# Performance work log

Hardware: AMD Instinct MI355X
Metric: run time of the kernel (lower is better)

The kernel has to match this reference:

```python
import jax, jax.numpy as jnp
import numpy as np

FACTOR = 2  # self.factor
KSIZE = 3   # causal_fusion depthwise conv kernel size


def causal_fusion(x, w, b):
    # x: [BH, C, N]; depthwise causal conv over the node axis (left pad k-1)
    k = w.shape[-1]
    out = jax.lax.conv_general_dilated(
        x, w, window_strides=(1,), padding=[(k - 1, 0)],
        dimension_numbers=('NCH', 'OIH', 'NCH'),
        feature_group_count=x.shape[1])
    return out + b[None, :, None]


def setup_inputs() -> dict:
    key = jax.random.key(0)
    ks = jax.random.split(key, 4)
    B, N, L, H, E = 4, 64, 128, 8, 32
    queries = jax.random.normal(ks[0], (B, N, L, H, E), jnp.float32)
    keys = jax.random.normal(ks[1], (B, N, L, H, E), jnp.float32)
    values = jax.random.normal(ks[2], (B, N, L, H, E), jnp.float32)
    attn_mask = jnp.zeros((1,), jnp.bool_)
    C = E * L  # 4096 channels seen by causal_fusion
    w_cf = jax.random.normal(ks[3], (C, 1, KSIZE), jnp.float32) * 0.05
    b_cf = jnp.zeros((C,), jnp.float32)
    return {"queries": queries, "keys": keys, "values": values,
            "attn_mask": attn_mask, "w_cf": w_cf, "b_cf": b_cf}


def reference(queries, keys, values, attn_mask, w_cf, b_cf):
    B, N, L, H, E = queries.shape  # S == L, so no pad/slice branch taken

    # --- FFT cross-correlation: corr[b,n,h,e,:] = irfft(rfft(mean_n q) * conj(rfft(k)))
    qm = jnp.broadcast_to(jnp.mean(queries, axis=1, keepdims=True), queries.shape)
    qp = jnp.transpose(qm, (0, 1, 3, 4, 2))      # [B,N,H,E,L]
    kp = jnp.transpose(keys, (0, 1, 3, 4, 2))    # [B,N,H,E,L]
    vp = jnp.transpose(values, (0, 1, 3, 4, 2))  # [B,N,H,E,L]
    corr = jnp.fft.irfft(jnp.fft.rfft(qp, axis=-1) * jnp.conj(jnp.fft.rfft(kp, axis=-1)), n=L, axis=-1)

    # --- align_speed: top-k delays over channel-mean corr, circular roll of values
    mean_corr = jnp.mean(corr, axis=3)                      # [B,N,H,L]
    weight, delay_idx = jax.lax.top_k(mean_corr, FACTOR)    # [B,N,H,F]
    delay = L - delay_idx                                   # values in [1, L]
    ar = jnp.arange(L)
    aligned = []
    for i in range(FACTOR):
        idx = (ar[None, None, None, None, :] + delay[..., i][..., None, None]) % L  # [B,N,H,1,L]
        idx = jnp.broadcast_to(idx, vp.shape)
        aligned.append(jnp.take_along_axis(vp, idx, axis=-1))  # [B,N,H,E,L]

    BH = B * H
    delay_bh = jnp.transpose(delay, (0, 2, 1, 3)).reshape(BH, N, FACTOR)
    weight_bh = jnp.transpose(weight, (0, 2, 1, 3)).reshape(BH, N, FACTOR)

    # --- per-factor: sort nodes by delay -> causal fusion over nodes -> unsort
    causal_agg = []
    for i in range(FACTOR):
        indices = jnp.argsort(delay_bh[..., i], axis=-1)               # [BH,N]
        av = jnp.transpose(aligned[i], (0, 2, 1, 3, 4)).reshape(BH, N, E, L)
        av = av * jax.nn.sigmoid(weight_bh[..., i])[:, :, None, None]
        sorted_av = jnp.take_along_axis(av, indices[:, :, None, None], axis=1)
        x = jnp.transpose(sorted_av.reshape(BH, N, E * L), (0, 2, 1))  # [BH,E*L,N]
        x = causal_fusion(x, w_cf, b_cf)
        x = jnp.transpose(x, (0, 2, 1)).reshape(BH, N, E, L)
        rev = jnp.argsort(indices, axis=-1)
        x = jnp.take_along_axis(x, rev[:, :, None, None], axis=1)
        causal_agg.append(jnp.transpose(x.reshape(B, H, N, E, L), (0, 2, 1, 3, 4)))  # [B,N,H,E,L]

    # --- align_back_speed: inverse circular shift, mean over factors
    delay_back = L - delay  # [B,N,H,F]
    agg = jnp.zeros_like(causal_agg[0])
    for i in range(FACTOR):
        idx = (ar[None, None, None, None, :] + delay_back[..., i][..., None, None]) % L
        idx = jnp.broadcast_to(idx, causal_agg[i].shape)
        agg = agg + jnp.take_along_axis(causal_agg[i], idx, axis=-1)
    agg = agg / FACTOR

    V = jnp.transpose(agg, (0, 1, 4, 2, 3))  # [B,N,L,H,E]
    return V
```

## Files before the change

### kernel.cpp

```cpp
#include <hip/hip_runtime.h>
#include <math.h>

#define B_ 4
#define N_ 64
#define L_ 128
#define H_ 8
#define E_ 32
#define SC_ 8

typedef __attribute__((ext_vector_type(8))) short short8;
typedef __attribute__((ext_vector_type(4))) float f32x4;

__device__ __forceinline__ unsigned short f2bf(float x) {
    union { float f; unsigned u; } c; c.f = x;
    unsigned r = (c.u + 0x7fffu + ((c.u >> 16) & 1u)) >> 16;
    return (unsigned short)r;
}
__device__ __forceinline__ float bf2f(unsigned short h) {
    union { unsigned u; float f; } c; c.u = ((unsigned)h) << 16;
    return c.f;
}

__global__ __launch_bounds__(256) void k_qmean(const float* __restrict__ q,
                                               float* __restrict__ qm,
                                               const float* __restrict__ w,
                                               const float* __restrict__ bias,
                                               float* __restrict__ wT,
                                               float* __restrict__ bT) {
    int blk = blockIdx.x;
    int b = blk >> 7, t = blk & 127;
    int tid = threadIdx.x;
    int c4 = tid & 63;
    int nq = tid >> 6;
    __shared__ double red[4][256];
    const f32x4* p = (const f32x4*)(q + (((size_t)(b * N_)) * L_ + t) * 256);
    double s0 = 0, s1 = 0, s2 = 0, s3 = 0;
    #pragma unroll 4
    for (int n = nq * 16; n < nq * 16 + 16; ++n) {
        f32x4 v = p[(size_t)n * 8192 + c4];
        s0 += (double)v.x; s1 += (double)v.y; s2 += (double)v.z; s3 += (double)v.w;
    }
    red[nq][c4 * 4 + 0] = s0;
    red[nq][c4 * 4 + 1] = s1;
    red[nq][c4 * 4 + 2] = s2;
    red[nq][c4 * 4 + 3] = s3;
    __syncthreads();
    int c = tid;
    double s = red[0][c] + red[1][c] + red[2][c] + red[3][c];
    qm[((size_t)b * 256 + c) * L_ + t] = (float)(s * (1.0 / 64.0));

    if (blk < 16) {
        int k = blk * 256 + tid;
        int e = k & 31, lp = k >> 5;
        int cc = e * L_ + lp;
        wT[k]        = w[cc * 3 + 0];
        wT[4096 + k] = w[cc * 3 + 1];
        wT[8192 + k] = w[cc * 3 + 2];
        bT[k]        = bias[cc];
    }
}

__global__ __launch_bounds__(512) void k_corr(const float* __restrict__ keys,
                                              const float* __restrict__ qm,
                                              float* __restrict__ part) {
    int blk = blockIdx.x;
    int sc = blk & 7; int bh = blk >> 3; int h = bh & 7; int b = bh >> 3;
    __shared__ unsigned short Ahi[4][64][40];
    __shared__ unsigned short Alo[4][64][40];
    __shared__ unsigned short Qhi[128][40];
    __shared__ unsigned short Qlo[128][40];
    int tid = threadIdx.x;
    int lane = tid & 63, w = tid >> 6;
    int mg = w & 1, ng = w >> 1;

    {
        int e = tid >> 4; int tq = (tid & 15) * 4;
        const float* qp = qm + ((size_t)b * 256 + h * 32 + e) * 128;
        #pragma unroll
        for (int hf = 0; hf < 2; ++hf) {
            int t0 = tq + hf * 64;
            float4 v = *(const float4*)(qp + t0);
            float vv[4] = {v.x, v.y, v.z, v.w};
            #pragma unroll
            for (int j = 0; j < 4; ++j) {
                unsigned short hi = f2bf(vv[j]);
                Qhi[t0 + j][e] = hi;
                Qlo[t0 + j][e] = f2bf(vv[j] - bf2f(hi));
            }
        }
    }
    int sn = tid >> 3; int se = (tid & 7) * 4;
    const float* kbase = keys + ((size_t)(b * N_ + sn) * L_) * 256 + h * 32 + se;
    #pragma unroll
    for (int p = 0; p < 2; ++p) {
        float4 v = *(const float4*)(kbase + (size_t)(sc * 16 + p) * 256);
        float vv[4] = {v.x, v.y, v.z, v.w};
        ushort4 h4, l4;
        unsigned short* hp = (unsigned short*)&h4;
        unsigned short* lp = (unsigned short*)&l4;
        #pragma unroll
        for (int j = 0; j < 4; ++j) {
            hp[j] = f2bf(vv[j]);
            lp[j] = f2bf(vv[j] - bf2f(hp[j]));
        }
        *(ushort4*)&Ahi[p][sn][se] = h4;
        *(ushort4*)&Alo[p][sn][se] = l4;
    }
    __syncthreads();

    f32x4 acc[2][2];
    #pragma unroll
    for (int i = 0; i < 2; ++i)
        #pragma unroll
        for (int j = 0; j < 2; ++j)
            acc[i][j] = (f32x4){0.f, 0.f, 0.f, 0.f};

    int eb = (lane >> 4) * 8;
    int rA0 = (mg * 2) * 16 + (lane & 15);
    int rA1 = rA0 + 16;
    int tau0 = (ng * 2) * 16 + (lane & 15);
    int tau1 = tau0 + 16;

    for (int it = 0; it < 8; ++it) {
        float4 stg0, stg1;
        if (it < 7) {
            stg0 = *(const float4*)(kbase + (size_t)(sc * 16 + 2 * it + 2) * 256);
            stg1 = *(const float4*)(kbase + (size_t)(sc * 16 + 2 * it + 3) * 256);
        }
        #pragma unroll
        for (int sp = 0; sp < 2; ++sp) {
            int p = 2 * it + sp;
            int slot = p & 3;
            int s = sc * 16 + p;
            short8 ah0 = *(const short8*)&Ahi[slot][rA0][eb];
            short8 ah1 = *(const short8*)&Ahi[slot][rA1][eb];
            short8 al0 = *(const short8*)&Alo[slot][rA0][eb];
            short8 al1 = *(const short8*)&Alo[slot][rA1][eb];
            int t0 = (s + tau0) & 127;
            int t1 = (s + tau1) & 127;
            short8 bh0 = *(const short8*)&Qhi[t0][eb];
            short8 bh1 = *(const short8*)&Qhi[t1][eb];
            short8 bl0 = *(const short8*)&Qlo[t0][eb];
            short8 bl1 = *(const short8*)&Qlo[t1][eb];
            acc[0][0] = __builtin_amdgcn_mfma_f32_16x16x32_bf16(ah0, bh0, acc[0][0], 0, 0, 0);
            acc[0][1] = __builtin_amdgcn_mfma_f32_16x16x32_bf16(ah0, bh1, acc[0][1], 0, 0, 0);
            acc[1][0] = __builtin_amdgcn_mfma_f32_16x16x32_bf16(ah1, bh0, acc[1][0], 0, 0, 0);
            acc[1][1] = __builtin_amdgcn_mfma_f32_16x16x32_bf16(ah1, bh1, acc[1][1], 0, 0, 0);
            acc[0][0] = __builtin_amdgcn_mfma_f32_16x16x32_bf16(ah0, bl0, acc[0][0], 0, 0, 0);
            acc[0][1] = __builtin_amdgcn_mfma_f32_16x16x32_bf16(ah0, bl1, acc[0][1], 0, 0, 0);
            acc[1][0] = __builtin_amdgcn_mfma_f32_16x16x32_bf16(ah1, bl0, acc[1][0], 0, 0, 0);
            acc[1][1] = __builtin_amdgcn_mfma_f32_16x16x32_bf16(ah1, bl1, acc[1][1], 0, 0, 0);
            acc[0][0] = __builtin_amdgcn_mfma_f32_16x16x32_bf16(al0, bh0, acc[0][0], 0, 0, 0);
            acc[0][1] = __builtin_amdgcn_mfma_f32_16x16x32_bf16(al0, bh1, acc[0][1], 0, 0, 0);
            acc[1][0] = __builtin_amdgcn_mfma_f32_16x16x32_bf16(al1, bh0, acc[1][0], 0, 0, 0);
            acc[1][1] = __builtin_amdgcn_mfma_f32_16x16x32_bf16(al1, bh1, acc[1][1], 0, 0, 0);
        }
        if (it < 7) {
            #pragma unroll
            for (int sp = 0; sp < 2; ++sp) {
                int p = 2 * it + 2 + sp;
                int slot = p & 3;
                float4 v = sp ? stg1 : stg0;
                float vv[4] = {v.x, v.y, v.z, v.w};
                ushort4 h4, l4;
                unsigned short* hp = (unsigned short*)&h4;
                unsigned short* lp = (unsigned short*)&l4;
                #pragma unroll
                for (int j = 0; j < 4; ++j) {
                    hp[j] = f2bf(vv[j]);
                    lp[j] = f2bf(vv[j] - bf2f(hp[j]));
                }
                *(ushort4*)&Ahi[slot][sn][se] = h4;
                *(ushort4*)&Alo[slot][sn][se] = l4;
            }
        }
        __syncthreads();
    }

    #pragma unroll
    for (int i = 0; i < 2; ++i) {
        int mt = mg * 2 + i;
        #pragma unroll
        for (int j = 0; j < 2; ++j) {
            int nt = ng * 2 + j;
            int tau = nt * 16 + (lane & 15);
            #pragma unroll
            for (int r = 0; r < 4; ++r) {
                int n = mt * 16 + (lane >> 4) * 4 + r;
                part[((((size_t)sc * B_ + b) * N_ + n) * H_ + h) * L_ + tau] = acc[i][j][r];
            }
        }
    }
}

__global__ __launch_bounds__(64) void k_topk(const float* __restrict__ part,
                                             int* __restrict__ didx,
                                             float* __restrict__ sig,
                                             int* __restrict__ flags) {
    int blk = blockIdx.x;
    int lane = threadIdx.x;
    size_t rb = (size_t)blk * L_;
    const size_t stride = (size_t)B_ * N_ * H_ * L_;
    double s0 = 0.0, s1 = 0.0;
    for (int sc = 0; sc < SC_; ++sc) {
        s0 += (double)part[sc * stride + rb + lane];
        s1 += (double)part[sc * stride + rb + lane + 64];
    }
    float v0 = (float)(s0 * (1.0 / 32.0));
    float v1 = (float)(s1 * (1.0 / 32.0));

    float bv = v0; int bi = lane;
    if (v1 > v0) { bv = v1; bi = lane + 64; }
    #pragma unroll
    for (int m = 32; m; m >>= 1) {
        float ov = __shfl_xor(bv, m, 64);
        int   oi = __shfl_xor(bi, m, 64);
        if (ov > bv || (ov == bv && oi < bi)) { bv = ov; bi = oi; }
    }
    int i1 = bi; float w1v = bv;

    float c0 = (lane == i1) ? -INFINITY : v0;
    float c1 = (lane + 64 == i1) ? -INFINITY : v1;
    float bv2 = c0; int bi2 = lane;
    if (c1 > c0) { bv2 = c1; bi2 = lane + 64; }
    #pragma unroll
    for (int m = 32; m; m >>= 1) {
        float ov = __shfl_xor(bv2, m, 64);
        int   oi = __shfl_xor(bi2, m, 64);
        if (ov > bv2 || (ov == bv2 && oi < bi2)) { bv2 = ov; bi2 = oi; }
    }
    int i2 = bi2; float w2v = bv2;

    float d0 = (lane == i1 || lane == i2) ? -INFINITY : v0;
    float d1 = (lane + 64 == i1 || lane + 64 == i2) ? -INFINITY : v1;
    float bv3 = fmaxf(d0, d1);
    #pragma unroll
    for (int m = 32; m; m >>= 1) bv3 = fmaxf(bv3, __shfl_xor(bv3, m, 64));

    if (lane == 0) {
        didx[blk * 2 + 0] = i1;
        didx[blk * 2 + 1] = i2;
        sig[blk * 2 + 0] = 1.f / (1.f + expf(-w1v));
        sig[blk * 2 + 1] = 1.f / (1.f + expf(-w2v));
        flags[blk] = (w2v - bv3 < 1e-3f) ? 1 : 0;
    }
}

__global__ __launch_bounds__(256) void k_fixup(const float* __restrict__ keys,
                                               const float* __restrict__ qm,
                                               const int* __restrict__ flags,
                                               double* __restrict__ vvg) {
    int row = blockIdx.x >> 3; int tg = blockIdx.x & 7;
    if (!flags[row]) return;
    int h = row & 7; int r = row >> 3; int n = r & 63; int b = r >> 6;
    __shared__ float ks_t[L_][E_];
    __shared__ float qs_t[L_][E_];
    __shared__ double red[16][17];
    int tid = threadIdx.x;
    for (int idx = tid; idx < 1024; idx += 256) {
        int s = idx >> 3, e4 = idx & 7;
        *(float4*)&ks_t[s][e4 * 4] =
            *(const float4*)&keys[(((size_t)(b * N_ + n)) * L_ + s) * 256 + h * E_ + e4 * 4];
        int e = idx >> 5, t4 = (idx & 31) * 4;
        float4 v = *(const float4*)&qm[((size_t)b * 256 + h * E_ + e) * L_ + t4];
        float vvj[4] = {v.x, v.y, v.z, v.w};
        #pragma unroll
        for (int j = 0; j < 4; ++j) {
            int t = t4 + j;
            int col = ((((e >> 2) ^ (t & 7)) << 2) | (e & 3));
            qs_t[t][col] = vvj[j];
        }
    }
    __syncthreads();
    int tau = tg * 16 + (tid & 15);
    int g = tid >> 4;
    double a0 = 0, a1 = 0, a2 = 0, a3 = 0, a4 = 0, a5 = 0, a6 = 0, a7 = 0;
    #pragma unroll 2
    for (int s = g * 8; s < g * 8 + 8; ++s) {
        int t = (s + tau) & 127;
        int x = t & 7;
        #pragma unroll
        for (int e4 = 0; e4 < 8; e4 += 2) {
            float4 k0 = *(const float4*)&ks_t[s][e4 * 4];
            float4 k1 = *(const float4*)&ks_t[s][e4 * 4 + 4];
            float4 q0 = *(const float4*)&qs_t[t][(e4 ^ x) << 2];
            float4 q1 = *(const float4*)&qs_t[t][((e4 + 1) ^ x) << 2];
            a0 = fma((double)k0.x, (double)q0.x, a0);
            a1 = fma((double)k0.y, (double)q0.y, a1);
            a2 = fma((double)k0.z, (double)q0.z, a2);
            a3 = fma((double)k0.w, (double)q0.w, a3);
            a4 = fma((double)k1.x, (double)q1.x, a4);
            a5 = fma((double)k1.y, (double)q1.y, a5);
            a6 = fma((double)k1.z, (double)q1.z, a6);
            a7 = fma((double)k1.w, (double)q1.w, a7);
        }
    }
    red[g][tid & 15] = ((a0 + a1) + (a2 + a3)) + ((a4 + a5) + (a6 + a7));
    __syncthreads();
    if (tid < 16) {
        double s = 0;
        #pragma unroll
        for (int gg = 0; gg < 16; ++gg) s += red[gg][tid];
        vvg[(size_t)row * L_ + tg * 16 + tid] = s;
    }
}

__global__ __launch_bounds__(128) void k_sort(int* __restrict__ didx,
                                              float* __restrict__ sig,
                                              const int* __restrict__ flags,
                                              const double* __restrict__ vvg,
                                              int* __restrict__ pred) {
    int bh = blockIdx.x;
    int b = bh >> 3, h = bh & 7;
    int tid = threadIdx.x; int i = tid >> 6; int n = tid & 63;
    __shared__ int ds[2][64];
    __shared__ int pm[2][64];
    ds[i][n] = 128 - didx[((b * 64 + n) * 8 + h) * 2 + i];
    __syncthreads();

    if (tid < 64) {
        int lane = tid;
        int myflag = flags[(b * 64 + lane) * 8 + h];
        unsigned long long msk = __ballot(myflag != 0);
        while (msk) {
            int nn = __ffsll((long long)msk) - 1; msk &= msk - 1;
            int row = (b * 64 + nn) * 8 + h;
            float v0 = (float)(vvg[(size_t)row * L_ + lane] * (1.0 / 32.0));
            float v1 = (float)(vvg[(size_t)row * L_ + lane + 64] * (1.0 / 32.0));
            float bv = v0; int bi = lane;
            if (v1 > v0) { bv = v1; bi = lane + 64; }
            #pragma unroll
            for (int m = 32; m; m >>= 1) {
                float ov = __shfl_xor(bv, m, 64);
                int   oi = __shfl_xor(bi, m, 64);
                if (ov > bv || (ov == bv && oi < bi)) { bv = ov; bi = oi; }
            }
            int i1 = bi; float w1v = bv;
            float c0 = (lane == i1) ? -INFINITY : v0;
            float c1 = (lane + 64 == i1) ? -INFINITY : v1;
            float bv2 = c0; int bi2 = lane;
            if (c1 > c0) { bv2 = c1; bi2 = lane + 64; }
            #pragma unroll
            for (int m = 32; m; m >>= 1) {
                float ov = __shfl_xor(bv2, m, 64);
                int   oi = __shfl_xor(bi2, m, 64);
                if (ov > bv2 || (ov == bv2 && oi < bi2)) { bv2 = ov; bi2 = oi; }
            }
            if (lane == 0) {
                didx[row * 2 + 0] = i1;
                didx[row * 2 + 1] = bi2;
                sig[row * 2 + 0] = 1.f / (1.f + expf(-w1v));
                sig[row * 2 + 1] = 1.f / (1.f + expf(-bv2));
                ds[0][nn] = 128 - i1;
                ds[1][nn] = 128 - bi2;
            }
        }
    }
    __syncthreads();

    int d = ds[i][n];
    int rank = 0;
    for (int m = 0; m < 64; ++m) {
        int dm = ds[i][m];
        rank += (dm < d || (dm == d && m < n)) ? 1 : 0;
    }
    pm[i][rank] = n;
    __syncthreads();
    int p1v = (rank >= 1) ? pm[i][rank - 1] : -1;
    int p2v = (rank >= 2) ? pm[i][rank - 2] : -1;
    int o = ((bh * 2 + i) * 64 + n) * 2;
    pred[o] = p1v; pred[o + 1] = p2v;
}

__global__ __launch_bounds__(256, 2) void k_out(const float* __restrict__ values,
                                                const float* __restrict__ wT,
                                                const float* __restrict__ bT,
                                                const int* __restrict__ didx,
                                                const float* __restrict__ sig,
                                                const int* __restrict__ pred,
                                                float* __restrict__ out) {
    int bid = blockIdx.x;
    int h = bid & 7;
    int b = bid >> 10;
    int j = (bid >> 3) & 127;
    int n = j >> 1; int half = j & 1;
    int blk = (b * 64 + n) * 8 + h;
    int tid = threadIdx.x; int e4 = tid & 7; int tq = tid >> 3;

    int di[2]; float si[2];
    int pq1[2], pq2[2], dq1[2], dq2[2]; float s1[2], s2[2];
    #pragma unroll
    for (int i = 0; i < 2; ++i) {
        di[i] = didx[blk * 2 + i];
        si[i] = sig[blk * 2 + i];
        int po = (((b * 8 + h) * 2 + i) * 64 + n) * 2;
        int p1 = pred[po], p2 = pred[po + 1];
        if (p1 >= 0) { int q = ((b * 64 + p1) * 8 + h) * 2 + i; pq1[i] = p1; dq1[i] = didx[q]; s1[i] = sig[q]; }
        else         { pq1[i] = n; dq1[i] = di[i]; s1[i] = 0.f; }
        if (p2 >= 0) { int q = ((b * 64 + p2) * 8 + h) * 2 + i; pq2[i] = p2; dq2[i] = didx[q]; s2[i] = sig[q]; }
        else         { pq2[i] = n; dq2[i] = di[i]; s2[i] = 0.f; }
    }
    const f32x4* v4 = (const f32x4*)values;
    const f32x4* w4 = (const f32x4*)wT;
    const f32x4* b4 = (const f32x4*)bT;
    f32x4* o4 = (f32x4*)out;
    const size_t base = ((size_t)b * N_) * L_ * 64 + h * 8 + e4;

    f32x4 vs[2], va1[2], va2[2], vb1[2], vb2[2];
    int lp0[2], lp1[2];
    #pragma unroll
    for (int it = 0; it < 2; ++it) {
        int t = half * 64 + tq + 32 * it;
        vs[it] = v4[base + ((size_t)n * L_ + t) * 64];
        int ta1 = (t + di[0] - dq1[0]) & 127;
        va1[it] = v4[base + ((size_t)pq1[0] * L_ + ta1) * 64];
        int ta2 = (t + di[0] - dq2[0]) & 127;
        va2[it] = v4[base + ((size_t)pq2[0] * L_ + ta2) * 64];
        int tb1 = (t + di[1] - dq1[1]) & 127;
        vb1[it] = v4[base + ((size_t)pq1[1] * L_ + tb1) * 64];
        int tb2 = (t + di[1] - dq2[1]) & 127;
        vb2[it] = v4[base + ((size_t)pq2[1] * L_ + tb2) * 64];
        lp0[it] = (t + di[0]) & 127;
        lp1[it] = (t + di[1]) & 127;
    }
    f32x4 bb0[2], w0a[2], w1a[2], w2a[2], bb1[2], w0b[2], w1b[2], w2b[2];
    #pragma unroll
    for (int it = 0; it < 2; ++it) {
        int wo0 = lp0[it] * 8 + e4, wo1 = lp1[it] * 8 + e4;
        bb0[it] = b4[wo0]; w0a[it] = w4[wo0]; w1a[it] = w4[1024 + wo0]; w2a[it] = w4[2048 + wo0];
        bb1[it] = b4[wo1]; w0b[it] = w4[wo1]; w1b[it] = w4[1024 + wo1]; w2b[it] = w4[2048 + wo1];
    }
    #pragma unroll
    for (int it = 0; it < 2; ++it) {
        int t = half * 64 + tq + 32 * it;
        f32x4 acc = bb0[it] + bb1[it];
        acc += w2a[it] * (si[0] * vs[it]);
        acc += w1a[it] * (s1[0] * va1[it]);
        acc += w0a[it] * (s2[0] * va2[it]);
        acc += w2b[it] * (si[1] * vs[it]);
        acc += w1b[it] * (s1[1] * vb1[it]);
        acc += w0b[it] * (s2[1] * vb2[it]);
        o4[base + ((size_t)n * L_ + t) * 64] = acc * 0.5f;
    }
}

extern "C" void kernel_launch(void* const* d_in, const int* in_sizes, int n_in,
                              void* d_out, int out_size, void* d_ws, size_t ws_size,
                              hipStream_t stream) {
    const float* queries = (const float*)d_in[0];
    const float* keys    = (const float*)d_in[1];
    const float* values  = (const float*)d_in[2];
    const float* w_cf = (const float*)d_in[4];
    const float* b_cf = (const float*)d_in[5];
    float* out = (float*)d_out;

    float* ws    = (float*)d_ws;
    float* qm    = ws;
    float* wT    = qm + 131072;
    float* bT    = wT + 12288;
    float* sigp  = bT + 4096;
    int*   didxp = (int*)(sigp + 4096);
    int*   predp = didxp + 4096;
    int*   flags = predp + 8192;
    double* vvg  = (double*)(flags + 2048);

    float* part = (float*)d_out;

    k_qmean <<<512,   256, 0, stream>>>(queries, qm, w_cf, b_cf, wT, bT);
    k_corr  <<<256,   512, 0, stream>>>(keys, qm, part);
    k_topk  <<<2048,  64,  0, stream>>>(part, didxp, sigp, flags);
    k_fixup <<<16384, 256, 0, stream>>>(keys, qm, flags, vvg);
    k_sort  <<<32,    128, 0, stream>>>(didxp, sigp, flags, vvg, predp);
    k_out   <<<4096,  256, 0, stream>>>(values, wT, bT, didxp, sigp, predp, out);
}
```

Baseline: 77.27 us.

## Compact fixup work via atomic worklist and precompute per-row gather params

k_topk now appends flagged rows to a global worklist through an atomic counter, and k_fixup runs as a persistent grid of 256 blocks that loops over that list. Previously 16384 blocks were launched and most exited early. k_sort now precomputes each row's predecessor indices, shift deltas and sigmoid weights into packed int4/float4 records, so k_out does one coalesced read per factor instead of chained dependent lookups. k_out is split into 8192 single-iteration blocks with a higher occupancy hint. The costs are an atomic per flagged row and a nondeterministic worklist order, though each vvg entry is still computed independently.

```diff
diff --git a/kernel.cpp b/kernel.cpp
--- a/kernel.cpp
+++ b/kernel.cpp
@@ -26,7 +26,8 @@
                                                const float* __restrict__ w,
                                                const float* __restrict__ bias,
                                                float* __restrict__ wT,
-                                               float* __restrict__ bT) {
+                                               float* __restrict__ bT,
+                                               int* __restrict__ wcnt) {
     int blk = blockIdx.x;
     int b = blk >> 7, t = blk & 127;
     int tid = threadIdx.x;
@@ -58,6 +59,7 @@
         wT[8192 + k] = w[cc * 3 + 2];
         bT[k]        = bias[cc];
     }
+    if (blk == 16 && tid == 0) *wcnt = 0;
 }
 
 __global__ __launch_bounds__(512) void k_corr(const float* __restrict__ keys,
@@ -196,7 +198,9 @@
 __global__ __launch_bounds__(64) void k_topk(const float* __restrict__ part,
                                              int* __restrict__ didx,
                                              float* __restrict__ sig,
-                                             int* __restrict__ flags) {
+                                             int* __restrict__ flags,
+                                             int* __restrict__ wlist,
+                                             int* __restrict__ wcnt) {
     int blk = blockIdx.x;
     int lane = threadIdx.x;
     size_t rb = (size_t)blk * L_;
@@ -242,80 +246,95 @@
         didx[blk * 2 + 1] = i2;
         sig[blk * 2 + 0] = 1.f / (1.f + expf(-w1v));
         sig[blk * 2 + 1] = 1.f / (1.f + expf(-w2v));
-        flags[blk] = (w2v - bv3 < 1e-3f) ? 1 : 0;
+        int fl = (w2v - bv3 < 1e-3f) ? 1 : 0;
+        flags[blk] = fl;
+        if (fl) { int s = atomicAdd(wcnt, 1); wlist[s] = blk; }
     }
 }
 
 __global__ __launch_bounds__(256) void k_fixup(const float* __restrict__ keys,
                                                const float* __restrict__ qm,
-                                               const int* __restrict__ flags,
+                                               const int* __restrict__ wlist,
+                                               const int* __restrict__ wcnt,
                                                double* __restrict__ vvg) {
-    int row = blockIdx.x >> 3; int tg = blockIdx.x & 7;
-    if (!flags[row]) return;
-    int h = row & 7; int r = row >> 3; int n = r & 63; int b = r >> 6;
+    int cnt = *wcnt;
     __shared__ float ks_t[L_][E_];
     __shared__ float qs_t[L_][E_];
     __shared__ double red[16][17];
     int tid = threadIdx.x;
-    for (int idx = tid; idx < 1024; idx += 256) {
-        int s = idx >> 3, e4 = idx & 7;
-        *(float4*)&ks_t[s][e4 * 4] =
-            *(const float4*)&keys[(((size_t)(b * N_ + n)) * L_ + s) * 256 + h * E_ + e4 * 4];
-        int e = idx >> 5, t4 = (idx & 31) * 4;
-        float4 v = *(const float4*)&qm[((size_t)b * 256 + h * E_ + e) * L_ + t4];
-        float vvj[4] = {v.x, v.y, v.z, v.w};
-        #pragma unroll
-        for (int j = 0; j < 4; ++j) {
-            int t = t4 + j;
-            int col = ((((e >> 2) ^ (t & 7)) << 2) | (e & 3));
-            qs_t[t][col] = vvj[j];
-        }
-    }
-    __syncthreads();
-    int tau = tg * 16 + (tid & 15);
-    int g = tid >> 4;
-    double a0 = 0, a1 = 0, a2 = 0, a3 = 0, a4 = 0, a5 = 0, a6 = 0, a7 = 0;
-    #pragma unroll 2
-    for (int s = g * 8; s < g * 8 + 8; ++s) {
-        int t = (s + tau) & 127;
-        int x = t & 7;
-        #pragma unroll
-        for (int e4 = 0; e4 < 8; e4 += 2) {
-            float4 k0 = *(const float4*)&ks_t[s][e4 * 4];
-            float4 k1 = *(const float4*)&ks_t[s][e4 * 4 + 4];
-            float4 q0 = *(const float4*)&qs_t[t][(e4 ^ x) << 2];
-            float4 q1 = *(const float4*)&qs_t[t][((e4 + 1) ^ x) << 2];
-            a0 = fma((double)k0.x, (double)q0.x, a0);
-            a1 = fma((double)k0.y, (double)q0.y, a1);
-            a2 = fma((double)k0.z, (double)q0.z, a2);
-            a3 = fma((double)k0.w, (double)q0.w, a3);
-            a4 = fma((double)k1.x, (double)q1.x, a4);
-            a5 = fma((double)k1.y, (double)q1.y, a5);
-            a6 = fma((double)k1.z, (double)q1.z, a6);
-            a7 = fma((double)k1.w, (double)q1.w, a7);
-        }
-    }
-    red[g][tid & 15] = ((a0 + a1) + (a2 + a3)) + ((a4 + a5) + (a6 + a7));
-    __syncthreads();
-    if (tid < 16) {
-        double s = 0;
-        #pragma unroll
-        for (int gg = 0; gg < 16; ++gg) s += red[gg][tid];
-        vvg[(size_t)row * L_ + tg * 16 + tid] = s;
-    }
-}
-
-__global__ __launch_bounds__(128) void k_sort(int* __restrict__ didx,
-                                              float* __restrict__ sig,
+    for (int wi = blockIdx.x; wi < cnt * 8; wi += gridDim.x) {
+        int row = wlist[wi >> 3]; int tg = wi & 7;
+        int h = row & 7; int r = row >> 3; int n = r & 63; int b = r >> 6;
+        __syncthreads();
+        for (int idx = tid; idx < 1024; idx += 256) {
+            int s = idx >> 3, e4 = idx & 7;
+            *(float4*)&ks_t[s][e4 * 4] =
+                *(const float4*)&keys[(((size_t)(b * N_ + n)) * L_ + s) * 256 + h * E_ + e4 * 4];
+            int e = idx >> 5, t4 = (idx & 31) * 4;
+            float4 v = *(const float4*)&qm[((size_t)b * 256 + h * E_ + e) * L_ + t4];
+            float vvj[4] = {v.x, v.y, v.z, v.w};
+            #pragma unroll
+            for (int j = 0; j < 4; ++j) {
+                int t = t4 + j;
+                int col = ((((e >> 2) ^ (t & 7)) << 2) | (e & 3));
+                qs_t[t][col] = vvj[j];
+            }
+        }
+        __syncthreads();
+        int tau = tg * 16 + (tid & 15);
+        int g = tid >> 4;
+        double a0 = 0, a1 = 0, a2 = 0, a3 = 0, a4 = 0, a5 = 0, a6 = 0, a7 = 0;
+        #pragma unroll 2
+        for (int s = g * 8; s < g * 8 + 8; ++s) {
+            int t = (s + tau) & 127;
+            int x = t & 7;
+            #pragma unroll
+            for (int e4 = 0; e4 < 8; e4 += 2) {
+                float4 k0 = *(const float4*)&ks_t[s][e4 * 4];
+                float4 k1 = *(const float4*)&ks_t[s][e4 * 4 + 4];
+                float4 q0 = *(const float4*)&qs_t[t][(e4 ^ x) << 2];
+                float4 q1 = *(const float4*)&qs_t[t][((e4 + 1) ^ x) << 2];
+                a0 = fma((double)k0.x, (double)q0.x, a0);
+                a1 = fma((double)k0.y, (double)q0.y, a1);
+                a2 = fma((double)k0.z, (double)q0.z, a2);
+                a3 = fma((double)k0.w, (double)q0.w, a3);
+                a4 = fma((double)k1.x, (double)q1.x, a4);
+                a5 = fma((double)k1.y, (double)q1.y, a5);
+                a6 = fma((double)k1.z, (double)q1.z, a6);
+                a7 = fma((double)k1.w, (double)q1.w, a7);
+            }
+        }
+        red[g][tid & 15] = ((a0 + a1) + (a2 + a3)) + ((a4 + a5) + (a6 + a7));
+        __syncthreads();
+        if (tid < 16) {
+            double s = 0;
+            #pragma unroll
+            for (int gg = 0; gg < 16; ++gg) s += red[gg][tid];
+            vvg[(size_t)row * L_ + tg * 16 + tid] = s;
+        }
+    }
+}
+
+__global__ __launch_bounds__(128) void k_sort(const int* __restrict__ didx,
+                                              const float* __restrict__ sig,
                                               const int* __restrict__ flags,
                                               const double* __restrict__ vvg,
-                                              int* __restrict__ pred) {
+                                              int4* __restrict__ gparam_i,
+                                              f32x4* __restrict__ gparam_f) {
     int bh = blockIdx.x;
     int b = bh >> 3, h = bh & 7;
     int tid = threadIdx.x; int i = tid >> 6; int n = tid & 63;
     __shared__ int ds[2][64];
     __shared__ int pm[2][64];
-    ds[i][n] = 128 - didx[((b * 64 + n) * 8 + h) * 2 + i];
+    __shared__ int dival[2][64];
+    __shared__ float sigval[2][64];
+    {
+        int row = (b * 64 + n) * 8 + h;
+        int dv = didx[row * 2 + i];
+        dival[i][n] = dv;
+        sigval[i][n] = sig[row * 2 + i];
+        ds[i][n] = 128 - dv;
+    }
     __syncthreads();
 
     if (tid < 64) {
@@ -347,12 +366,10 @@
                 if (ov > bv2 || (ov == bv2 && oi < bi2)) { bv2 = ov; bi2 = oi; }
             }
             if (lane == 0) {
-                didx[row * 2 + 0] = i1;
-                didx[row * 2 + 1] = bi2;
-                sig[row * 2 + 0] = 1.f / (1.f + expf(-w1v));
-                sig[row * 2 + 1] = 1.f / (1.f + expf(-bv2));
-                ds[0][nn] = 128 - i1;
-                ds[1][nn] = 128 - bi2;
+                dival[0][nn] = i1;      ds[0][nn] = 128 - i1;
+                dival[1][nn] = bi2;     ds[1][nn] = 128 - bi2;
+                sigval[0][nn] = 1.f / (1.f + expf(-w1v));
+                sigval[1][nn] = 1.f / (1.f + expf(-bv2));
             }
         }
     }
@@ -368,80 +385,64 @@
     __syncthreads();
     int p1v = (rank >= 1) ? pm[i][rank - 1] : -1;
     int p2v = (rank >= 2) ? pm[i][rank - 2] : -1;
-    int o = ((bh * 2 + i) * 64 + n) * 2;
-    pred[o] = p1v; pred[o + 1] = p2v;
-}
-
-__global__ __launch_bounds__(256, 2) void k_out(const float* __restrict__ values,
+
+    int din = dival[i][n];
+    int pq1 = (p1v >= 0) ? p1v : n;
+    int pq2 = (p2v >= 0) ? p2v : n;
+    int d1 = (p1v >= 0) ? ((din - dival[i][p1v]) & 127) : 0;
+    int d2 = (p2v >= 0) ? ((din - dival[i][p2v]) & 127) : 0;
+    float s1 = (p1v >= 0) ? sigval[i][p1v] : 0.f;
+    float s2 = (p2v >= 0) ? sigval[i][p2v] : 0.f;
+    int blko = (b * 64 + n) * 8 + h;
+    gparam_i[blko * 2 + i] = make_int4(pq1, pq2, d1, d2);
+    gparam_f[blko * 2 + i] = (f32x4){s1, s2, sigval[i][n], (float)din};
+}
+
+__global__ __launch_bounds__(256, 3) void k_out(const float* __restrict__ values,
                                                 const float* __restrict__ wT,
                                                 const float* __restrict__ bT,
-                                                const int* __restrict__ didx,
-                                                const float* __restrict__ sig,
-                                                const int* __restrict__ pred,
+                                                const int4* __restrict__ gparam_i,
+                                                const f32x4* __restrict__ gparam_f,
                                                 float* __restrict__ out) {
     int bid = blockIdx.x;
     int h = bid & 7;
-    int b = bid >> 10;
-    int j = (bid >> 3) & 127;
-    int n = j >> 1; int half = j & 1;
+    int q = (bid >> 3) & 3;
+    int n = (bid >> 5) & 63;
+    int b = bid >> 11;
     int blk = (b * 64 + n) * 8 + h;
     int tid = threadIdx.x; int e4 = tid & 7; int tq = tid >> 3;
-
-    int di[2]; float si[2];
-    int pq1[2], pq2[2], dq1[2], dq2[2]; float s1[2], s2[2];
-    #pragma unroll
-    for (int i = 0; i < 2; ++i) {
-        di[i] = didx[blk * 2 + i];
-        si[i] = sig[blk * 2 + i];
-        int po = (((b * 8 + h) * 2 + i) * 64 + n) * 2;
-        int p1 = pred[po], p2 = pred[po + 1];
-        if (p1 >= 0) { int q = ((b * 64 + p1) * 8 + h) * 2 + i; pq1[i] = p1; dq1[i] = didx[q]; s1[i] = sig[q]; }
-        else         { pq1[i] = n; dq1[i] = di[i]; s1[i] = 0.f; }
-        if (p2 >= 0) { int q = ((b * 64 + p2) * 8 + h) * 2 + i; pq2[i] = p2; dq2[i] = didx[q]; s2[i] = sig[q]; }
-        else         { pq2[i] = n; dq2[i] = di[i]; s2[i] = 0.f; }
-    }
+    int t = q * 32 + tq;
+
+    int4  gi0 = gparam_i[blk * 2 + 0];
+    int4  gi1 = gparam_i[blk * 2 + 1];
+    f32x4 gf0 = gparam_f[blk * 2 + 0];
+    f32x4 gf1 = gparam_f[blk * 2 + 1];
+    int di0 = (int)gf0.w, di1 = (int)gf1.w;
+
     const f32x4* v4 = (const f32x4*)values;
     const f32x4* w4 = (const f32x4*)wT;
     const f32x4* b4 = (const f32x4*)bT;
     f32x4* o4 = (f32x4*)out;
     const size_t base = ((size_t)b * N_) * L_ * 64 + h * 8 + e4;
 
-    f32x4 vs[2], va1[2], va2[2], vb1[2], vb2[2];
-    int lp0[2], lp1[2];
-    #pragma unroll
-    for (int it = 0; it < 2; ++it) {
-        int t = half * 64 + tq + 32 * it;
-        vs[it] = v4[base + ((size_t)n * L_ + t) * 64];
-        int ta1 = (t + di[0] - dq1[0]) & 127;
-        va1[it] = v4[base + ((size_t)pq1[0] * L_ + ta1) * 64];
-        int ta2 = (t + di[0] - dq2[0]) & 127;
-        va2[it] = v4[base + ((size_t)pq2[0] * L_ + ta2) * 64];
-        int tb1 = (t + di[1] - dq1[1]) & 127;
-        vb1[it] = v4[base + ((size_t)pq1[1] * L_ + tb1) * 64];
-        int tb2 = (t + di[1] - dq2[1]) & 127;
-        vb2[it] = v4[base + ((size_t)pq2[1] * L_ + tb2) * 64];
-        lp0[it] = (t + di[0]) & 127;
-        lp1[it] = (t + di[1]) & 127;
-    }
-    f32x4 bb0[2], w0a[2], w1a[2], w2a[2], bb1[2], w0b[2], w1b[2], w2b[2];
-    #pragma unroll
-    for (int it = 0; it < 2; ++it) {
-        int wo0 = lp0[it] * 8 + e4, wo1 = lp1[it] * 8 + e4;
-        bb0[it] = b4[wo0]; w0a[it] = w4[wo0]; w1a[it] = w4[1024 + wo0]; w2a[it] = w4[2048 + wo0];
-        bb1[it] = b4[wo1]; w0b[it] = w4[wo1]; w1b[it] = w4[1024 + wo1]; w2b[it] = w4[2048 + wo1];
-    }
-    #pragma unroll
-    for (int it = 0; it < 2; ++it) {
-        int t = half * 64 + tq + 32 * it;
-        f32x4 acc = bb0[it] + bb1[it];
-        acc += w2a[it] * (si[0] * vs[it]);
-        acc += w1a[it] * (s1[0] * va1[it]);
-        acc += w0a[it] * (s2[0] * va2[it]);
-        acc += w2b[it] * (si[1] * vs[it]);
-        acc += w1b[it] * (s1[1] * vb1[it]);
-        acc += w0b[it] * (s2[1] * vb2[it]);
-        o4[base + ((size_t)n * L_ + t) * 64] = acc * 0.5f;
-    }
+    f32x4 vs  = v4[base + ((size_t)n * L_ + t) * 64];
+    f32x4 va1 = v4[base + ((size_t)gi0.x * L_ + ((t + gi0.z) & 127)) * 64];
+    f32x4 va2 = v4[base + ((size_t)gi0.y * L_ + ((t + gi0.w) & 127)) * 64];
+    f32x4 vb1 = v4[base + ((size_t)gi1.x * L_ + ((t + gi1.z) & 127)) * 64];
+    f32x4 vb2 = v4[base + ((size_t)gi1.y * L_ + ((t + gi1.w) & 127)) * 64];
+    int wo0 = ((t + di0) & 127) * 8 + e4;
+    int wo1 = ((t + di1) & 127) * 8 + e4;
+    f32x4 bb0 = b4[wo0], w0a = w4[wo0], w1a = w4[1024 + wo0], w2a = w4[2048 + wo0];
+    f32x4 bb1 = b4[wo1], w0b = w4[wo1], w1b = w4[1024 + wo1], w2b = w4[2048 + wo1];
+
+    f32x4 acc = bb0 + bb1;
+    acc += w2a * (gf0.z * vs);
+    acc += w1a * (gf0.x * va1);
+    acc += w0a * (gf0.y * va2);
+    acc += w2b * (gf1.z * vs);
+    acc += w1b * (gf1.x * vb1);
+    acc += w0b * (gf1.y * vb2);
+    o4[base + ((size_t)n * L_ + t) * 64] = acc * 0.5f;
 }
 
 extern "C" void kernel_launch(void* const* d_in, const int* in_sizes, int n_in,
@@ -460,16 +461,19 @@
     float* bT    = wT + 12288;
     float* sigp  = bT + 4096;
     int*   didxp = (int*)(sigp + 4096);
-    int*   predp = didxp + 4096;
-    int*   flags = predp + 8192;
-    double* vvg  = (double*)(flags + 2048);
+    int*   flags = didxp + 4096;
+    int*   wlist = flags + 2048;
+    int*   wcnt  = wlist + 2048;
+    double* vvg  = (double*)(wcnt + 4);
+    int4*  gpi   = (int4*)(vvg + 2048 * 128);
+    f32x4* gpf   = (f32x4*)(gpi + 4096);
 
     float* part = (float*)d_out;
 
-    k_qmean <<<512,   256, 0, stream>>>(queries, qm, w_cf, b_cf, wT, bT);
-    k_corr  <<<256,   512, 0, stream>>>(keys, qm, part);
-    k_topk  <<<2048,  64,  0, stream>>>(part, didxp, sigp, flags);
-    k_fixup <<<16384, 256, 0, stream>>>(keys, qm, flags, vvg);
-    k_sort  <<<32,    128, 0, stream>>>(didxp, sigp, flags, vvg, predp);
-    k_out   <<<4096,  256, 0, stream>>>(values, wT, bT, didxp, sigp, predp, out);
-}
+    k_qmean <<<512,  256, 0, stream>>>(queries, qm, w_cf, b_cf, wT, bT, wcnt);
+    k_corr  <<<256,  512, 0, stream>>>(keys, qm, part);
+    k_topk  <<<2048, 64,  0, stream>>>(part, didxp, sigp, flags, wlist, wcnt);
+    k_fixup <<<256,  256, 0, stream>>>(keys, qm, wlist, wcnt, vvg);
+    k_sort  <<<32,   128, 0, stream>>>(didxp, sigp, flags, vvg, gpi, gpf);
+    k_out   <<<8192, 256, 0, stream>>>(values, wT, bT, gpi, gpf, out);
+}
```

Result: faster. 71.97 us (-6.9%).
